# Performance work log

Hardware: AMD Instinct MI355X
Metric: run time of the kernel (lower is better)

Reference implementation:

```python
import jax, jax.numpy as jnp
import numpy as np

B, IN, H, F, T = 4096, 1024, 1024, 128, 3
LN_EPS = 1e-5


def setup_inputs() -> dict:
    key = jax.random.key(0)
    ks = jax.random.split(key, 12)
    inp = {
        "input_": jax.random.normal(ks[0], (B, IN), jnp.float32),
        "hx": jax.random.normal(ks[1], (B, H), jnp.float32),
        "cx": jax.random.normal(ks[2], (B, H), jnp.float32),
        "topic_w": jax.random.uniform(ks[3], (B, T), jnp.float32),
        # factorized gate weights (init scales per reset_parameters)
        "w_ih_a": jax.random.normal(ks[4], (4 * H, F), jnp.float32) / jnp.sqrt(F),
        "w_ih_b": jnp.full((F, T), 0.1 / T, jnp.float32),
        "w_ih_c": jax.random.normal(ks[5], (F, IN), jnp.float32) / jnp.sqrt(IN),
        "w_hh_a": 0.1 * jax.random.normal(ks[6], (4 * H, F), jnp.float32),
        "w_hh_b": jnp.full((F, T), 0.1 / T, jnp.float32),
        "w_hh_c": 0.1 * jax.random.normal(ks[7], (F, H), jnp.float32),
        # theta transforms: weight=0, bias=1 per reset_parameters
        "th_ih_w": jnp.zeros((T, T), jnp.float32),
        "th_ih_b": jnp.ones((T,), jnp.float32),
        "th_hh_w": jnp.zeros((T, T), jnp.float32),
        "th_hh_b": jnp.ones((T,), jnp.float32),
        # layernorm params
        "ln_i_w": jnp.ones((4 * H,), jnp.float32),
        "ln_i_b": jnp.zeros((4 * H,), jnp.float32),
        "ln_h_w": jnp.ones((4 * H,), jnp.float32),
        "ln_h_b": jnp.zeros((4 * H,), jnp.float32),
        "ln_c_w": jnp.ones((H,), jnp.float32),
        "ln_c_b": jnp.zeros((H,), jnp.float32),
    }
    return inp


def _ln(x, w, b):
    mu = x.mean(-1, keepdims=True)
    var = ((x - mu) ** 2).mean(-1, keepdims=True)
    return (x - mu) * jax.lax.rsqrt(var + LN_EPS) * w + b


def reference(input_, hx, cx, topic_w,
              w_ih_a, w_ih_b, w_ih_c, w_hh_a, w_hh_b, w_hh_c,
              th_ih_w, th_ih_b, th_hh_w, th_hh_b,
              ln_i_w, ln_i_b, ln_h_w, ln_h_b, ln_c_w, ln_c_b):
    # factorized input gates: ((x @ C^T) * (theta(topic) @ B^T)) @ A^T
    scale_i = (topic_w @ th_ih_w.T + th_ih_b) @ w_ih_b.T            # [B, F]
    igates = ((input_ @ w_ih_c.T) * scale_i) @ w_ih_a.T             # [B, 4H]
    scale_h = (topic_w @ th_hh_w.T + th_hh_b) @ w_hh_b.T            # [B, F]
    hgates = ((hx @ w_hh_c.T) * scale_h) @ w_hh_a.T                 # [B, 4H]

    gates = _ln(igates, ln_i_w, ln_i_b) + _ln(hgates, ln_h_w, ln_h_b)
    i, f, g, o = jnp.split(gates, 4, axis=1)
    i = jax.nn.sigmoid(i)
    f = jax.nn.sigmoid(f)
    g = jnp.tanh(g)  # dropout p=0 -> identity
    o = jax.nn.sigmoid(o)
    cy = _ln(f * cx + i * g, ln_c_w, ln_c_b)
    hy = o * jnp.tanh(cy)
    return hy, cy
```

## Files before the change

kernel.cpp:

```cpp
#include <hip/hip_runtime.h>

typedef unsigned short ushort_t;
typedef __attribute__((ext_vector_type(8))) short bf8_t;
typedef __attribute__((ext_vector_type(4))) float f4_t;

#define B_   4096
#define IN_  1024
#define H_   1024
#define F_   128
#define G4_  4096
#define EPS_ 1e-5f

#define NG1   512
#define NPREP 256
#define NGRAM 128

__device__ __forceinline__ float us2f(unsigned short s) {
  union { unsigned int u; float f; } v;
  v.u = ((unsigned int)s) << 16;
  return v.f;
}
__device__ __forceinline__ unsigned short f2us(float f) {
  union { float f; unsigned int u; } v;
  v.f = f;
  unsigned int r = (v.u + 0x7fffu + ((v.u >> 16) & 1u)) >> 16;
  return (unsigned short)r;
}
__device__ __forceinline__ float sigf(float x) { return 1.0f / (1.0f + __expf(-x)); }
__device__ __forceinline__ float tanh_f(float x) { return 1.0f - 2.0f / (1.0f + __expf(2.0f * x)); }

__device__ __forceinline__ int detect_fp32(const void* disc) {
  return ((const unsigned int*)disc)[0] == 0x3F800000u;
}
__device__ __forceinline__ float ldf(const void* p, int i, int fp32) {
  return fp32 ? ((const float*)p)[i] : us2f(((const ushort_t*)p)[i]);
}
__device__ __forceinline__ void ld8(const void* p, int idx, float* o, int fp32) {
  if (fp32) {
    const float4* q = (const float4*)((const float*)p + idx);
    float4 v0 = q[0], v1 = q[1];
    o[0]=v0.x; o[1]=v0.y; o[2]=v0.z; o[3]=v0.w;
    o[4]=v1.x; o[5]=v1.y; o[6]=v1.z; o[7]=v1.w;
  } else {
    uint4 v = *(const uint4*)((const ushort_t*)p + idx);
    const ushort_t* pv = (const ushort_t*)&v;
    #pragma unroll
    for (int i = 0; i < 8; i++) o[i] = us2f(pv[i]);
  }
}
__device__ __forceinline__ bf8_t cvt8p(const float* f) {
  union { bf8_t v; unsigned int u[4]; } r;
  const unsigned int* ui = (const unsigned int*)f;
  #pragma unroll
  for (int i = 0; i < 4; i++) {
    unsigned int lo = ui[2 * i] + 0x8000u;
    unsigned int hi = ui[2 * i + 1] + 0x8000u;
    r.u[i] = __builtin_amdgcn_perm(hi, lo, 0x07060302u);
  }
  return r.v;
}

__global__ __launch_bounds__(256, 4) void k_stageA(
    const void* __restrict__ X0, const void* __restrict__ X1,
    const void* __restrict__ Wc0, const void* __restrict__ Wc1,
    const void* __restrict__ topic,
    const void* __restrict__ thw0, const void* __restrict__ thw1,
    const void* __restrict__ thb0, const void* __restrict__ thb1,
    const void* __restrict__ wsb0, const void* __restrict__ wsb1,
    const void* __restrict__ Ai, const void* __restrict__ Ah,
    const void* __restrict__ lnwi, const void* __restrict__ lnwh,
    ushort_t* __restrict__ wb,
    float* __restrict__ cm_i, float* __restrict__ cm_h,
    float* __restrict__ g_i, float* __restrict__ g_h,
    float* __restrict__ C0, float* __restrict__ C1)
{
  __shared__ float smem[32 * 128];
  int bid = blockIdx.x, tid = threadIdx.x;
  int fp32 = detect_fp32(lnwi);

  if (bid < NG1) {
    int rb = bid >> 1, mat = bid & 1;
    const void* X   = mat ? X1 : X0;
    const void* W   = mat ? Wc1 : Wc0;
    const void* thw = mat ? thw1 : thw0;
    const void* thb = mat ? thb1 : thb0;
    const void* wbp = mat ? wsb1 : wsb0;
    float* C = mat ? C1 : C0;
    int lane = tid & 63, w = tid >> 6;
    int quad = lane >> 4, lcol = lane & 15;
    int brow0 = rb * 16;

    f4_t acc[2];
    acc[0] = (f4_t){0.f, 0.f, 0.f, 0.f};
    acc[1] = (f4_t){0.f, 0.f, 0.f, 0.f};

    #pragma unroll 4
    for (int kc = 0; kc < 32; kc++) {
      int kb = kc * 32 + quad * 8;
      float a[8];
      ld8(X, (brow0 + lcol) * IN_ + kb, a, fp32);
      bf8_t af = cvt8p(a);
      #pragma unroll
      for (int t = 0; t < 2; t++) {
        float bt[8];
        ld8(W, ((w * 2 + t) * 16 + lcol) * IN_ + kb, bt, fp32);
        acc[t] = __builtin_amdgcn_mfma_f32_16x16x32_bf16(af, cvt8p(bt), acc[t], 0, 0, 0);
      }
    }

    float thwf[3][3], thbf[3];
    #pragma unroll
    for (int t = 0; t < 3; t++) {
      thbf[t] = ldf(thb, t, fp32);
      #pragma unroll
      for (int t2 = 0; t2 < 3; t2++) thwf[t][t2] = ldf(thw, t * 3 + t2, fp32);
    }
    float tmpv[4][3];
    #pragma unroll
    for (int reg = 0; reg < 4; reg++) {
      int b = brow0 + quad * 4 + reg;
      float tp0 = ldf(topic, b * 3 + 0, fp32);
      float tp1 = ldf(topic, b * 3 + 1, fp32);
      float tp2 = ldf(topic, b * 3 + 2, fp32);
      #pragma unroll
      for (int t = 0; t < 3; t++)
        tmpv[reg][t] = thbf[t] + tp0 * thwf[t][0] + tp1 * thwf[t][1] + tp2 * thwf[t][2];
    }
    #pragma unroll
    for (int t = 0; t < 2; t++) {
      int f = (w * 2 + t) * 16 + lcol;
      float wv0 = ldf(wbp, f * 3 + 0, fp32);
      float wv1 = ldf(wbp, f * 3 + 1, fp32);
      float wv2 = ldf(wbp, f * 3 + 2, fp32);
      #pragma unroll
      for (int reg = 0; reg < 4; reg++) {
        float sc = tmpv[reg][0] * wv0 + tmpv[reg][1] * wv1 + tmpv[reg][2] * wv2;
        C[(brow0 + quad * 4 + reg) * F_ + f] = acc[t][reg] * sc;
      }
    }
  } else if (bid < NG1 + NPREP) {
    int t = bid - NG1;
    #pragma unroll
    for (int i = 0; i < 16; i++) {
      int e = i * 256 + tid;
      int c = e >> 9, l = (e >> 3) & 63, j = e & 7;
      int k = c * 32 + ((l >> 4) << 3) + j;
      int n = t * 16 + (l & 15);
      float v;
      if (k < 128) v = ldf(Ai, n * F_ + k, fp32) * ldf(lnwi, n, fp32);
      else         v = ldf(Ah, n * F_ + (k - 128), fp32) * ldf(lnwh, n, fp32);
      wb[(size_t)t * 4096 + e] = f2us(v);
    }
    const void* A = (tid < 128) ? Ai : Ah;
    float* cm = (tid < 128) ? cm_i : cm_h;
    int f = tid & 127;
    float s = 0.f;
    #pragma unroll
    for (int i = 0; i < 16; i++) s += ldf(A, (t * 16 + i) * F_ + f, fp32);
    atomicAdd(&cm[f], s);
  } else {
    int g = bid - (NG1 + NPREP);
    int fblk = g & 3, mat = (g >> 2) & 1, z = g >> 3;
    const void* A = mat ? Ah : Ai;
    float* G = mat ? g_h : g_i;
    float (*As)[128] = (float(*)[128])smem;
    int f1_0 = fblk * 32;
    int tf2 = tid & 31, tf1 = tid >> 5;
    float acc[4][4] = {};
    int nbase = z * 256;
    for (int n0 = nbase; n0 < nbase + 256; n0 += 32) {
      #pragma unroll
      for (int j = 0; j < 2; j++) {
        int idx = tid + 256 * j;
        int nn = idx >> 4, f8 = (idx & 15) * 8;
        float t[8];
        ld8(A, (n0 + nn) * F_ + f8, t, fp32);
        #pragma unroll
        for (int i = 0; i < 8; i++) As[nn][f8 + i] = t[i];
      }
      __syncthreads();
      #pragma unroll 4
      for (int nn = 0; nn < 32; nn++) {
        float4 a1 = *(const float4*)&As[nn][f1_0 + 4 * tf1];
        float4 a2 = *(const float4*)&As[nn][4 * tf2];
        const float* x1 = (const float*)&a1;
        const float* x2 = (const float*)&a2;
        #pragma unroll
        for (int i = 0; i < 4; i++)
          #pragma unroll
          for (int j = 0; j < 4; j++) acc[i][j] += x1[i] * x2[j];
      }
      __syncthreads();
    }
    #pragma unroll
    for (int i = 0; i < 4; i++)
      #pragma unroll
      for (int j = 0; j < 4; j++)
        atomicAdd(&G[(f1_0 + 4 * tf1 + i) * F_ + 4 * tf2 + j], acc[i][j]);
  }
}

__global__ __launch_bounds__(256, 4) void k_stats2(
    const float* __restrict__ C0, const float* __restrict__ C1,
    const float* __restrict__ g_i, const float* __restrict__ g_h,
    const float* __restrict__ cm_i, const float* __restrict__ cm_h,
    float* __restrict__ mrs_i, float* __restrict__ mrs_h,
    ushort_t* __restrict__ xb)
{
  int bid = blockIdx.x;
  int rb = bid >> 1, mat = bid & 1;
  const float* C  = mat ? C1 : C0;
  const float* G  = mat ? g_h : g_i;
  const float* cm = mat ? cm_h : cm_i;
  float* mrs = mat ? mrs_h : mrs_i;
  int kbase = mat ? 128 : 0;

  int tid = threadIdx.x;
  int lane = tid & 63, w = tid >> 6;
  int quad = lane >> 4, lcol = lane & 15;
  int b0 = rb * 16;

  __shared__ float p1part[4][16];
  __shared__ float p2s[16];
  __shared__ float rs_s[16];

  bf8_t af[4];
  float p2p = 0.f;
  #pragma unroll
  for (int kc = 0; kc < 4; kc++) {
    int kb = kc * 32 + quad * 8;
    const float4* q = (const float4*)(C + (b0 + lcol) * F_ + kb);
    float4 v0 = q[0], v1 = q[1];
    float a[8] = {v0.x, v0.y, v0.z, v0.w, v1.x, v1.y, v1.z, v1.w};
    af[kc] = cvt8p(a);
    if (w == 0) {
      #pragma unroll
      for (int j = 0; j < 8; j++) p2p += a[j] * cm[kb + j];
    }
  }

  float p1p[4] = {0.f, 0.f, 0.f, 0.f};
  #pragma unroll
  for (int t = 0; t < 2; t++) {
    int colf = (w * 2 + t) * 16 + lcol;
    f4_t acc = {0.f, 0.f, 0.f, 0.f};
    #pragma unroll
    for (int kc = 0; kc < 4; kc++) {
      const float4* qg = (const float4*)(G + colf * F_ + kc * 32 + quad * 8);
      float4 w0 = qg[0], w1 = qg[1];
      float bt[8] = {w0.x, w0.y, w0.z, w0.w, w1.x, w1.y, w1.z, w1.w};
      acc = __builtin_amdgcn_mfma_f32_16x16x32_bf16(af[kc], cvt8p(bt), acc, 0, 0, 0);
    }
    #pragma unroll
    for (int reg = 0; reg < 4; reg++)
      p1p[reg] += acc[reg] * C[(b0 + quad * 4 + reg) * F_ + colf];
  }
  #pragma unroll
  for (int d = 1; d < 16; d <<= 1)
    #pragma unroll
    for (int reg = 0; reg < 4; reg++)
      p1p[reg] += __shfl_xor(p1p[reg], d, 64);
  if (lcol == 0) {
    #pragma unroll
    for (int reg = 0; reg < 4; reg++)
      p1part[w][quad * 4 + reg] = p1p[reg];
  }
  if (w == 0) {
    p2p += __shfl_xor(p2p, 16, 64);
    p2p += __shfl_xor(p2p, 32, 64);
    if (quad == 0) p2s[lcol] = p2p;
  }
  __syncthreads();
  if (tid < 16) {
    float p1 = p1part[0][tid] + p1part[1][tid] + p1part[2][tid] + p1part[3][tid];
    float E2 = p1 * (1.0f / 4096.0f);
    float mu = p2s[tid] * (1.0f / 4096.0f);
    float var = E2 - mu * mu;
    float rs = rsqrtf(var + EPS_);
    rs_s[tid] = rs;
    mrs[b0 + tid] = mu * rs;
  }
  __syncthreads();
  int f = tid & 127, half = tid >> 7;
  ushort_t* xbb = xb + (size_t)rb * 4096;
  int k = kbase + f;
  int c = k >> 5, lq = (k >> 3) & 3, j = k & 7;
  #pragma unroll
  for (int i = 0; i < 8; i++) {
    int r2 = half * 8 + i;
    int lfrag = r2 | (lq << 4);
    xbb[c * 512 + lfrag * 8 + j] = f2us(C[(b0 + r2) * F_ + f] * rs_s[r2]);
  }
}

__global__ __launch_bounds__(1024) void k_fused(
    const ushort_t* __restrict__ xb, const ushort_t* __restrict__ wb,
    const float* __restrict__ mrs_i, const float* __restrict__ mrs_h,
    const void* __restrict__ lniw, const void* __restrict__ lnib,
    const void* __restrict__ lnhw, const void* __restrict__ lnhb,
    const void* __restrict__ lncw, const void* __restrict__ lncb,
    const void* __restrict__ cx, float* __restrict__ out)
{
  __shared__ float buf[16][1028];
  __shared__ float obuf[16][1028];
  __shared__ ushort_t xs[4096];
  __shared__ float wpart[16][16][2];
  __shared__ float mu_s[16], rs_s[16];
  int tid = threadIdx.x;
  int lane = tid & 63, w = tid >> 6;
  int quad = lane >> 4, lcol = lane & 15;
  int b0 = blockIdx.x * 16;
  int fp32 = detect_fp32(lniw);

  ((unsigned long long*)xs)[tid] =
      ((const unsigned long long*)(xb + (size_t)blockIdx.x * 4096))[tid];

  float mi[4], mh[4];
  #pragma unroll
  for (int reg = 0; reg < 4; reg++) {
    mi[reg] = mrs_i[b0 + quad * 4 + reg];
    mh[reg] = mrs_h[b0 + quad * 4 + reg];
  }
  __syncthreads();

  float s1[4] = {0.f, 0.f, 0.f, 0.f}, s2[4] = {0.f, 0.f, 0.f, 0.f};

  #pragma unroll
  for (int q = 0; q < 4; q++) {
    int cg = w * 4 + q;
    int col = cg * 16 + lcol;
    float cxv[4];
    #pragma unroll
    for (int reg = 0; reg < 4; reg++)
      cxv[reg] = ldf(cx, (size_t)(b0 + quad * 4 + reg) * H_ + col, fp32);

    f4_t accg[4];
    #pragma unroll
    for (int g = 0; g < 4; g++) accg[g] = (f4_t){0.f, 0.f, 0.f, 0.f};
    #pragma unroll
    for (int c = 0; c < 8; c++) {
      bf8_t af = *(const bf8_t*)&xs[c * 512 + lane * 8];
      #pragma unroll
      for (int g = 0; g < 4; g++) {
        bf8_t bf = *(const bf8_t*)(wb + (size_t)(g * 64 + cg) * 4096 + c * 512 + lane * 8);
        accg[g] = __builtin_amdgcn_mfma_f32_16x16x32_bf16(af, bf, accg[g], 0, 0, 0);
      }
    }
    float liw0 = ldf(lniw, 0 * H_ + col, fp32), lib0 = ldf(lnib, 0 * H_ + col, fp32);
    float lhw0 = ldf(lnhw, 0 * H_ + col, fp32), lhb0 = ldf(lnhb, 0 * H_ + col, fp32);
    float liw1 = ldf(lniw, 1 * H_ + col, fp32), lib1 = ldf(lnib, 1 * H_ + col, fp32);
    float lhw1 = ldf(lnhw, 1 * H_ + col, fp32), lhb1 = ldf(lnhb, 1 * H_ + col, fp32);
    float liw2 = ldf(lniw, 2 * H_ + col, fp32), lib2 = ldf(lnib, 2 * H_ + col, fp32);
    float lhw2 = ldf(lnhw, 2 * H_ + col, fp32), lhb2 = ldf(lnhb, 2 * H_ + col, fp32);
    float liw3 = ldf(lniw, 3 * H_ + col, fp32), lib3 = ldf(lnib, 3 * H_ + col, fp32);
    float lhw3 = ldf(lnhw, 3 * H_ + col, fp32), lhb3 = ldf(lnhb, 3 * H_ + col, fp32);
    #pragma unroll
    for (int reg = 0; reg < 4; reg++) {
      int m = quad * 4 + reg;
      float gi = accg[0][reg] + lib0 + lhb0 - mi[reg] * liw0 - mh[reg] * lhw0;
      float gf = accg[1][reg] + lib1 + lhb1 - mi[reg] * liw1 - mh[reg] * lhw1;
      float gg = accg[2][reg] + lib2 + lhb2 - mi[reg] * liw2 - mh[reg] * lhw2;
      float go = accg[3][reg] + lib3 + lhb3 - mi[reg] * liw3 - mh[reg] * lhw3;
      float iv = sigf(gi), fv = sigf(gf), gv = tanh_f(gg), ov = sigf(go);
      float cval = fv * cxv[reg] + iv * gv;
      buf[m][col] = cval;
      obuf[m][col] = ov;
      s1[reg] += cval;
      s2[reg] += cval * cval;
    }
  }

  #pragma unroll
  for (int d = 1; d < 16; d <<= 1) {
    #pragma unroll
    for (int reg = 0; reg < 4; reg++) {
      s1[reg] += __shfl_xor(s1[reg], d, 64);
      s2[reg] += __shfl_xor(s2[reg], d, 64);
    }
  }
  if (lcol == 0) {
    #pragma unroll
    for (int reg = 0; reg < 4; reg++) {
      wpart[w][quad * 4 + reg][0] = s1[reg];
      wpart[w][quad * 4 + reg][1] = s2[reg];
    }
  }
  __syncthreads();
  if (tid < 16) {
    float t1 = 0.f, t2 = 0.f;
    #pragma unroll
    for (int ww = 0; ww < 16; ww++) { t1 += wpart[ww][tid][0]; t2 += wpart[ww][tid][1]; }
    float mu = t1 * (1.0f / 1024.0f);
    float var = t2 * (1.0f / 1024.0f) - mu * mu;
    mu_s[tid] = mu;
    rs_s[tid] = rsqrtf(var + EPS_);
  }
  __syncthreads();

  #pragma unroll
  for (int q = 0; q < 4; q++) {
    int col = (w * 4 + q) * 16 + lcol;
    float lw = ldf(lncw, col, fp32), lb = ldf(lncb, col, fp32);
    #pragma unroll
    for (int reg = 0; reg < 4; reg++) {
      int m = quad * 4 + reg;
      float cyv = (buf[m][col] - mu_s[m]) * rs_s[m] * lw + lb;
      out[(size_t)B_ * H_ + (size_t)(b0 + m) * H_ + col] = cyv;
      out[(size_t)(b0 + m) * H_ + col] = obuf[m][col] * tanh_f(cyv);
    }
  }
}

extern "C" void kernel_launch(void* const* d_in, const int* in_sizes, int n_in,
                              void* d_out, int out_size, void* d_ws, size_t ws_size,
                              hipStream_t stream) {
  const void* input_  = d_in[0];
  const void* hx      = d_in[1];
  const void* cx      = d_in[2];
  const void* topic   = d_in[3];
  const void* w_ih_a  = d_in[4];
  const void* w_ih_b  = d_in[5];
  const void* w_ih_c  = d_in[6];
  const void* w_hh_a  = d_in[7];
  const void* w_hh_b  = d_in[8];
  const void* w_hh_c  = d_in[9];
  const void* th_ih_w = d_in[10];
  const void* th_ih_b = d_in[11];
  const void* th_hh_w = d_in[12];
  const void* th_hh_b = d_in[13];
  const void* ln_i_w  = d_in[14];
  const void* ln_i_b  = d_in[15];
  const void* ln_h_w  = d_in[16];
  const void* ln_h_b  = d_in[17];
  const void* ln_c_w  = d_in[18];
  const void* ln_c_b  = d_in[19];

  float* w = (float*)d_ws;
  float* c1    = w;
  float* c2    = c1 + B_ * F_;
  float* g_i   = c2 + B_ * F_;
  float* g_h   = g_i + F_ * F_;
  float* cm_i  = g_h + F_ * F_;
  float* cm_h  = cm_i + F_;
  float* mrs_i = cm_h + F_;
  float* mrs_h = mrs_i + B_;
  ushort_t* xb = (ushort_t*)(mrs_h + B_);
  ushort_t* wbf = xb + (size_t)B_ * 256;

  hipMemsetAsync(g_i, 0, (size_t)(2 * F_ * F_ + 2 * F_) * sizeof(float), stream);

  k_stageA<<<dim3(NG1 + NPREP + NGRAM), dim3(256), 0, stream>>>(
      input_, hx, w_ih_c, w_hh_c, topic,
      th_ih_w, th_hh_w, th_ih_b, th_hh_b, w_ih_b, w_hh_b,
      w_ih_a, w_hh_a, ln_i_w, ln_h_w,
      wbf, cm_i, cm_h, g_i, g_h, c1, c2);
  k_stats2<<<dim3(512), dim3(256), 0, stream>>>(
      c1, c2, g_i, g_h, cm_i, cm_h, mrs_i, mrs_h, xb);
  k_fused<<<dim3(256), dim3(1024), 0, stream>>>(
      xb, wbf, mrs_i, mrs_h,
      ln_i_w, ln_i_b, ln_h_w, ln_h_b, ln_c_w, ln_c_b, cx, (float*)d_out);
}
```

Baseline: 226.3 us.

## Stage X tile in swizzled LDS and double-buffer W loads in stage A GEMM

The stage-A projection GEMM now loads the block's 16-row X tile once into XOR-swizzled LDS as bf16, where previously the four waves each re-read it from global memory. It also software-pipelines the W fragment loads with two register buffers so that global loads overlap the MFMAs. The shared buffer grows to 32 KB and is reused by the Gram branch. This raises LDS use and register pressure, which could lower occupancy under launch_bounds(256,4).

```diff
diff --git a/kernel.cpp b/kernel.cpp
--- a/kernel.cpp
+++ b/kernel.cpp
@@ -74,7 +74,7 @@
     float* __restrict__ g_i, float* __restrict__ g_h,
     float* __restrict__ C0, float* __restrict__ C1)
 {
-  __shared__ float smem[32 * 128];
+  __shared__ __align__(16) char lds_raw[32768];
   int bid = blockIdx.x, tid = threadIdx.x;
   int fp32 = detect_fp32(lnwi);
 
@@ -90,23 +90,49 @@
     int quad = lane >> 4, lcol = lane & 15;
     int brow0 = rb * 16;
 
+    #pragma unroll
+    for (int p = 0; p < 8; p++) {
+      int fl = p * 2048 + tid * 8;
+      int r = fl >> 10, cidx = fl & 1023;
+      float t8[8];
+      ld8(X, (brow0 + r) * IN_ + cidx, t8, fp32);
+      bf8_t v = cvt8p(t8);
+      int byte = (r * 2048 + cidx * 2) ^ ((r & 7) << 4);
+      *(bf8_t*)(lds_raw + byte) = v;
+    }
+    __syncthreads();
+
     f4_t acc[2];
     acc[0] = (f4_t){0.f, 0.f, 0.f, 0.f};
     acc[1] = (f4_t){0.f, 0.f, 0.f, 0.f};
 
-    #pragma unroll 4
-    for (int kc = 0; kc < 32; kc++) {
-      int kb = kc * 32 + quad * 8;
-      float a[8];
-      ld8(X, (brow0 + lcol) * IN_ + kb, a, fp32);
-      bf8_t af = cvt8p(a);
-      #pragma unroll
-      for (int t = 0; t < 2; t++) {
-        float bt[8];
-        ld8(W, ((w * 2 + t) * 16 + lcol) * IN_ + kb, bt, fp32);
-        acc[t] = __builtin_amdgcn_mfma_f32_16x16x32_bf16(af, cvt8p(bt), acc[t], 0, 0, 0);
-      }
-    }
+    int wrow = w * 32 + lcol;
+    int quad8 = quad * 8;
+    int afbase = lcol * 2048 + quad * 16;
+    int afxor = (lcol & 7) << 4;
+
+#define AF_(kc) (*(const bf8_t*)(lds_raw + ((afbase + (kc) * 64) ^ afxor)))
+#define LOADW_(buf, kc) { \
+      ld8(W, (wrow)      * IN_ + (kc) * 32 + quad8, buf[0], fp32); \
+      ld8(W, (wrow + 16) * IN_ + (kc) * 32 + quad8, buf[1], fp32); }
+#define STEPK_(buf, kc) { \
+      bf8_t af_ = AF_(kc); \
+      acc[0] = __builtin_amdgcn_mfma_f32_16x16x32_bf16(af_, cvt8p(buf[0]), acc[0], 0, 0, 0); \
+      acc[1] = __builtin_amdgcn_mfma_f32_16x16x32_bf16(af_, cvt8p(buf[1]), acc[1], 0, 0, 0); }
+
+    float pb0[2][8], pb1[2][8];
+    LOADW_(pb0, 0);
+    LOADW_(pb1, 1);
+    #pragma unroll
+    for (int kc = 0; kc < 32; kc += 2) {
+      STEPK_(pb0, kc);
+      if (kc + 2 < 32) LOADW_(pb0, kc + 2);
+      STEPK_(pb1, kc + 1);
+      if (kc + 3 < 32) LOADW_(pb1, kc + 3);
+    }
+#undef AF_
+#undef LOADW_
+#undef STEPK_
 
     float thwf[3][3], thbf[3];
     #pragma unroll
@@ -163,7 +189,7 @@
     int fblk = g & 3, mat = (g >> 2) & 1, z = g >> 3;
     const void* A = mat ? Ah : Ai;
     float* G = mat ? g_h : g_i;
-    float (*As)[128] = (float(*)[128])smem;
+    float (*As)[128] = (float(*)[128])lds_raw;
     int f1_0 = fblk * 32;
     int tf2 = tid & 31, tf1 = tid >> 5;
     float acc[4][4] = {};
```

Result: faster. 216.2 us (-4.5%).
